# Kernel optimization log

Hardware: AMD Instinct MI355X
Metric: run time of the kernel (lower is better)

Reference implementation:

```python
import jax, jax.numpy as jnp
import numpy as np

NUM_BINS = 8
TAIL = 3.0
MBW = 1e-3
MBH = 1e-3
MD = 1e-3


def _conv(x, w, b):
    y = jax.lax.conv_general_dilated(x, w, (1, 1), 'SAME',
                                     dimension_numbers=('NCHW', 'OIHW', 'NCHW'))
    return y + b[None, :, None, None]


def _rqs_forward(x, uw, uh, ud):
    # x: [N]; uw/uh: [N,K]; ud: [N,K-1]. Linear tails at |x|>TAIL.
    K = NUM_BINS
    inside = (x >= -TAIL) & (x <= TAIL)
    pad_const = float(np.log(np.expm1(1.0 - MD)))
    ud = jnp.pad(ud, ((0, 0), (1, 1)), constant_values=pad_const)  # [N,K+1]

    w = MBW + (1.0 - MBW * K) * jax.nn.softmax(uw, axis=-1)
    cw = jnp.pad(jnp.cumsum(w, axis=-1), ((0, 0), (1, 0)))
    cw = 2.0 * TAIL * cw - TAIL
    cw = cw.at[:, 0].set(-TAIL).at[:, -1].set(TAIL)
    w = cw[:, 1:] - cw[:, :-1]

    h = MBH + (1.0 - MBH * K) * jax.nn.softmax(uh, axis=-1)
    ch = jnp.pad(jnp.cumsum(h, axis=-1), ((0, 0), (1, 0)))
    ch = 2.0 * TAIL * ch - TAIL
    ch = ch.at[:, 0].set(-TAIL).at[:, -1].set(TAIL)
    h = ch[:, 1:] - ch[:, :-1]

    d = MD + jax.nn.softplus(ud)  # [N,K+1]

    xc = jnp.clip(x, -TAIL, TAIL)
    idx = jnp.clip(jnp.sum(xc[:, None] >= cw, axis=-1) - 1, 0, K - 1)[:, None]
    g = lambda a, i: jnp.take_along_axis(a, i, axis=1)[:, 0]
    icw, iw = g(cw, idx), g(w, idx)
    ich, ih = g(ch, idx), g(h, idx)
    idl, idr = g(d, idx), g(d, idx + 1)

    delta = ih / iw
    th = (xc - icw) / iw
    th1 = 1.0 - th
    num = ih * (delta * th * th + idl * th * th1)
    den = delta + (idl + idr - 2.0 * delta) * th * th1
    y = ich + num / den
    dnum = delta * delta * (idr * th * th + 2.0 * delta * th * th1 + idl * th1 * th1)
    lad = jnp.log(dnum) - 2.0 * jnp.log(den)
    return jnp.where(inside, y, x), jnp.where(inside, lad, 0.0)


def _checker_mask(H, W):
    # parity=0: zeros at (even,even) and (odd,odd) -> mask = (i+j) % 2
    m = (np.add.outer(np.arange(H), np.arange(W)) % 2).astype(np.float32)
    return jnp.asarray(m)[None, None]


def setup_inputs() -> dict:
    key = jax.random.key(0)
    ks = jax.random.split(key, 6)
    B, C, H, W = 16, 12, 128, 128
    hid, c_out = 128, 12 * (3 * NUM_BINS - 1)  # 276
    return {
        'x': jax.random.normal(ks[0], (B, C, H, W), jnp.float32),
        'logdet': jnp.zeros((B,), jnp.float32),
        'conditioning': jax.random.normal(ks[1], (B, 4, H, W), jnp.float32),
        'w1': jax.random.normal(ks[2], (hid, C + 4, 3, 3), jnp.float32) * 0.05,
        'b1': jnp.zeros((hid,), jnp.float32),
        'w2': jax.random.normal(ks[3], (hid, hid, 3, 3), jnp.float32) * 0.05,
        'b2': jnp.zeros((hid,), jnp.float32),
        'w3': jax.random.normal(ks[4], (c_out, hid, 3, 3), jnp.float32) * 0.05,
        'b3': jnp.zeros((c_out,), jnp.float32),
    }


def reference(x, logdet, conditioning, w1, b1, w2, b2, w3, b3):
    B, C, H, W = x.shape
    K = NUM_BINS
    mask = _checker_mask(H, W)
    x_frozen = mask * x
    x_active = (1.0 - mask) * x

    inp = jnp.concatenate([x_frozen, conditioning], axis=1)
    hdn = jax.nn.relu(_conv(inp, w1, b1))
    hdn = jax.nn.relu(_conv(hdn, w2, b2))
    params = _conv(hdn, w3, b3)  # [B, C*(3K-1), H, W]

    params = params.reshape(B, C, 3 * K - 1, H, W).transpose(0, 1, 3, 4, 2)
    params = params.reshape(B * C * H * W, 3 * K - 1)
    uw, uh, ud = params[:, :K], params[:, K:2 * K], params[:, 2 * K:]

    y_flat, lad_flat = _rqs_forward(x_active.reshape(-1), uw, uh, ud)
    y = y_flat.reshape(B, C, H, W)
    x_out = x_frozen + y * (1.0 - mask)
    lad = lad_flat.reshape(B, C, H, W) * (1.0 - mask)
    return x_out, logdet + lad.sum(axis=(1, 2, 3))
```

## Files before the change

kernel.cpp:

```cpp
#include <hip/hip_runtime.h>
#include <hip/hip_bf16.h>
#include <math.h>

constexpr int B_ = 16, C_ = 12, H_ = 128, W_ = 128, HID = 128;
constexpr float TAILF = 3.0f, MBWF = 0.001f, MBHF = 0.001f, MDF = 0.001f;

typedef __attribute__((ext_vector_type(8))) short bf16x8;
typedef __attribute__((ext_vector_type(4))) short bf16x4;
typedef __attribute__((ext_vector_type(4))) float f32x4;
typedef __attribute__((ext_vector_type(2))) float f32x2;

__device__ __forceinline__ float softplusf(float v) {
    return (v > 20.f) ? v : log1pf(expf(v));
}
__device__ __forceinline__ short bf16bits(float v) {
    __hip_bfloat16 t = __float2bfloat16(v);
    return *reinterpret_cast<short*>(&t);
}
__device__ __forceinline__ float bf2f(short s) {
    __hip_bfloat16 t = *reinterpret_cast<__hip_bfloat16*>(&s);
    return __bfloat162float(t);
}

__global__ void pack_w1_kern(const float* __restrict__ w1,
                             __hip_bfloat16* __restrict__ wp) {
    int e = blockIdx.x * 256 + threadIdx.x;
    int j = e & 7, lane = (e >> 3) & 63, mt = (e >> 9) & 7;
    int chunk = e >> 12;
    int oc = mt * 16 + (lane & 15);
    int k_local = (lane >> 4) * 8 + j;
    int kpos = 2 * chunk + (k_local >> 4);
    int ic = k_local & 15;
    float v = (kpos < 9) ? w1[(oc * 16 + ic) * 9 + kpos] : 0.f;
    wp[e] = __float2bfloat16(v);
}

__global__ void pack_w2_kern(const float* __restrict__ w2,
                             __hip_bfloat16* __restrict__ wp) {
    int e = blockIdx.x * 256 + threadIdx.x;
    int j = e & 7, lane = (e >> 3) & 63, mt = (e >> 9) & 7;
    int chunk = (e >> 12) & 3, kpos = e >> 14;
    int oc = mt * 16 + (lane & 15);
    int ic = chunk * 32 + (lane >> 4) * 8 + j;
    wp[e] = __float2bfloat16(w2[(oc * 128 + ic) * 9 + kpos]);
}

__global__ void pack_w3_kern(const float* __restrict__ w3,
                             __hip_bfloat16* __restrict__ wp) {
    int e = blockIdx.x * 256 + threadIdx.x;
    int j = e & 7, lane = (e >> 3) & 63;
    int rest = e >> 9;
    int mt = rest % 24; rest /= 24;
    int chunk = rest & 3, kpos = rest >> 2;
    int ocp = mt * 16 + (lane & 15);
    int c = ocp / 24, jp = ocp % 24;
    int ic = chunk * 32 + (lane >> 4) * 8 + j;
    float v = 0.f;
    if (ocp < 288 && jp < 23)
        v = w3[((c * 23 + jp) * 128 + ic) * 9 + kpos];
    wp[e] = __float2bfloat16(v);
}

__global__ __launch_bounds__(256) void conv1_mfma_kern(
    const float* __restrict__ x, const float* __restrict__ cond,
    const __hip_bfloat16* __restrict__ wp1,
    const float* __restrict__ b1,
    __hip_bfloat16* __restrict__ h1)
{
    const int tile = blockIdx.x & 255;
    const int b    = blockIdx.x >> 8;
    const int h0 = (tile >> 4) << 3;
    const int w0 = (tile & 15) << 3;
    const int tid = threadIdx.x;
    const int wv = tid >> 6, l = tid & 63;
    const int lg = l >> 4, ln = l & 15;

    __shared__ __hip_bfloat16 sB[100 * 20];

    for (int e = tid; e < 1600; e += 256) {
        int ch = e / 100, pos = e % 100;
        int ph = pos / 10, pw = pos % 10;
        int gh = h0 + ph - 1, gw = w0 + pw - 1;
        float v = 0.f;
        if (gh >= 0 && gh < H_ && gw >= 0 && gw < W_) {
            if (ch < 12) {
                v = ((gh + gw) & 1) ? x[((b * C_ + ch) * H_ + gh) * W_ + gw] : 0.f;
            } else {
                v = cond[((b * 4 + (ch - 12)) * H_ + gh) * W_ + gw];
            }
        }
        sB[pos * 20 + ch] = __float2bfloat16(v);
    }
    __syncthreads();

    f32x4 acc[2][4];
#pragma unroll
    for (int mi = 0; mi < 2; ++mi) {
        const int ocbase = (wv * 2 + mi) * 16 + lg * 4;
#pragma unroll
        for (int nt = 0; nt < 4; ++nt)
#pragma unroll
            for (int r = 0; r < 4; ++r)
                acc[mi][nt][r] = b1[ocbase + r];
    }

#pragma unroll
    for (int chunk = 0; chunk < 5; ++chunk) {
        const int kpos = (chunk == 4) ? 8 : (2 * chunk + (lg >> 1));
        const int kh = kpos / 3, kw = kpos % 3;
        bf16x8 afr[2];
#pragma unroll
        for (int mi = 0; mi < 2; ++mi)
            afr[mi] = *reinterpret_cast<const bf16x8*>(
                &wp1[(size_t)((chunk * 8 + wv * 2 + mi) * 64 + l) * 8]);
        bf16x8 bfr[4];
#pragma unroll
        for (int nt = 0; nt < 4; ++nt) {
            int px = nt * 16 + ln;
            int pos = ((px >> 3) + kh) * 10 + (px & 7) + kw;
            bfr[nt] = *reinterpret_cast<const bf16x8*>(&sB[pos * 20 + (lg & 1) * 8]);
        }
#pragma unroll
        for (int mi = 0; mi < 2; ++mi)
#pragma unroll
            for (int nt = 0; nt < 4; ++nt)
                acc[mi][nt] = __builtin_amdgcn_mfma_f32_16x16x32_bf16(
                    afr[mi], bfr[nt], acc[mi][nt], 0, 0, 0);
    }

#pragma unroll
    for (int mi = 0; mi < 2; ++mi) {
#pragma unroll
        for (int nt = 0; nt < 4; ++nt) {
            int px = nt * 16 + ln;
            int h = h0 + (px >> 3), w = w0 + (px & 7);
            bf16x4 o;
#pragma unroll
            for (int r = 0; r < 4; ++r)
                o[r] = bf16bits(fmaxf(acc[mi][nt][r], 0.f));
            *reinterpret_cast<bf16x4*>(
                &h1[(size_t)((b * H_ + h) * W_ + w) * HID + (wv * 2 + mi) * 16 + lg * 4]) = o;
        }
    }
}

__global__ __launch_bounds__(256) void conv2_mfma_kern(
    const __hip_bfloat16* __restrict__ h1,
    const __hip_bfloat16* __restrict__ wp2,
    const float* __restrict__ b2,
    __hip_bfloat16* __restrict__ h2)
{
    const int tile = blockIdx.x & 255;
    const int b    = blockIdx.x >> 8;
    const int h0 = (tile >> 4) << 3;
    const int w0 = (tile & 15) << 3;
    const int tid = threadIdx.x;
    const int wv = tid >> 6, l = tid & 63;
    const int lg = l >> 4, ln = l & 15;

    __shared__ __hip_bfloat16 sB[100 * 40];

    f32x4 acc[2][4];
#pragma unroll
    for (int mi = 0; mi < 2; ++mi) {
        const int ocbase = (wv * 2 + mi) * 16 + lg * 4;
#pragma unroll
        for (int nt = 0; nt < 4; ++nt)
#pragma unroll
            for (int r = 0; r < 4; ++r)
                acc[mi][nt][r] = b2[ocbase + r];
    }

    for (int chunk = 0; chunk < 4; ++chunk) {
        __syncthreads();
        for (int s = tid; s < 400; s += 256) {
            int pos = s >> 2, g = s & 3;
            int ph = pos / 10, pw = pos % 10;
            int gh = h0 + ph - 1, gw = w0 + pw - 1;
            bf16x8 v = {0, 0, 0, 0, 0, 0, 0, 0};
            if (gh >= 0 && gh < H_ && gw >= 0 && gw < W_)
                v = *reinterpret_cast<const bf16x8*>(
                    &h1[(size_t)((b * H_ + gh) * W_ + gw) * HID + chunk * 32 + g * 8]);
            *reinterpret_cast<bf16x8*>(&sB[pos * 40 + g * 8]) = v;
        }
        __syncthreads();
#pragma unroll
        for (int kpos = 0; kpos < 9; ++kpos) {
            const int kh = kpos / 3, kw = kpos % 3;
            bf16x8 afr[2];
#pragma unroll
            for (int mi = 0; mi < 2; ++mi)
                afr[mi] = *reinterpret_cast<const bf16x8*>(
                    &wp2[(size_t)(((kpos * 4 + chunk) * 8 + wv * 2 + mi) * 64 + l) * 8]);
            bf16x8 bfr[4];
#pragma unroll
            for (int nt = 0; nt < 4; ++nt) {
                int px = nt * 16 + ln;
                int pos = ((px >> 3) + kh) * 10 + (px & 7) + kw;
                bfr[nt] = *reinterpret_cast<const bf16x8*>(&sB[pos * 40 + lg * 8]);
            }
#pragma unroll
            for (int mi = 0; mi < 2; ++mi)
#pragma unroll
                for (int nt = 0; nt < 4; ++nt)
                    acc[mi][nt] = __builtin_amdgcn_mfma_f32_16x16x32_bf16(
                        afr[mi], bfr[nt], acc[mi][nt], 0, 0, 0);
        }
    }
#pragma unroll
    for (int mi = 0; mi < 2; ++mi) {
#pragma unroll
        for (int nt = 0; nt < 4; ++nt) {
            int px = nt * 16 + ln;
            int h = h0 + (px >> 3), w = w0 + (px & 7);
            bf16x4 o;
#pragma unroll
            for (int r = 0; r < 4; ++r)
                o[r] = bf16bits(fmaxf(acc[mi][nt][r], 0.f));
            *reinterpret_cast<bf16x4*>(
                &h2[(size_t)((b * H_ + h) * W_ + w) * HID + (wv * 2 + mi) * 16 + lg * 4]) = o;
        }
    }
}

__global__ __launch_bounds__(256) void conv3_gemm_kern(
    const __hip_bfloat16* __restrict__ h2,
    const __hip_bfloat16* __restrict__ wp3,
    const float* __restrict__ b3,
    __hip_bfloat16* __restrict__ park, int bbase)
{
    const int mblock = blockIdx.x % 3;
    const int t2 = blockIdx.x / 3;
    const int tile = t2 & 127;
    const int b8 = t2 >> 7;
    const int b = bbase + b8;
    const int r0 = (tile >> 4) << 4;
    const int w0 = (tile & 15) << 3;
    const int tid = threadIdx.x;
    const int wv = tid >> 6, l = tid & 63;
    const int lg = l >> 4, ln = l & 15;

    __shared__ __hip_bfloat16 sB[180 * 40];

    f32x4 acc[2][4];
#pragma unroll
    for (int mi = 0; mi < 2; ++mi) {
#pragma unroll
        for (int r = 0; r < 4; ++r) {
            int ocp = mblock * 128 + (wv * 2 + mi) * 16 + lg * 4 + r;
            int c = ocp / 24, jp = ocp % 24;
            float bv = (ocp < 288 && jp < 23) ? b3[c * 23 + jp] : 0.f;
#pragma unroll
            for (int nt = 0; nt < 4; ++nt) acc[mi][nt][r] = bv;
        }
    }

    for (int chunk = 0; chunk < 4; ++chunk) {
        __syncthreads();
        for (int s = tid; s < 720; s += 256) {
            int pos = s >> 2, g = s & 3;
            int ph = pos / 10, pw = pos % 10;
            int gh = r0 + ph - 1, gw = w0 + pw - 1;
            bf16x8 v = {0, 0, 0, 0, 0, 0, 0, 0};
            if (gh >= 0 && gh < H_ && gw >= 0 && gw < W_)
                v = *reinterpret_cast<const bf16x8*>(
                    &h2[(size_t)((b * H_ + gh) * W_ + gw) * HID + chunk * 32 + g * 8]);
            *reinterpret_cast<bf16x8*>(&sB[pos * 40 + g * 8]) = v;
        }
        __syncthreads();
#pragma unroll
        for (int kpos = 0; kpos < 9; ++kpos) {
            const int kh = kpos / 3, kw = kpos % 3;
            bf16x8 afr[2];
#pragma unroll
            for (int mi = 0; mi < 2; ++mi) {
                int mtg = mblock * 8 + wv * 2 + mi;
                afr[mi] = *reinterpret_cast<const bf16x8*>(
                    &wp3[(size_t)(((kpos * 4 + chunk) * 24 + mtg) * 64 + l) * 8]);
            }
            bf16x8 bfr[4];
#pragma unroll
            for (int nt = 0; nt < 4; ++nt) {
                int px = nt * 16 + ln;
                int rr = px >> 2, a = px & 3;
                int pos = (rr + kh) * 10 + 2 * a + (rr & 1) + kw;
                bfr[nt] = *reinterpret_cast<const bf16x8*>(&sB[pos * 40 + lg * 8]);
            }
#pragma unroll
            for (int mi = 0; mi < 2; ++mi)
#pragma unroll
                for (int nt = 0; nt < 4; ++nt)
                    acc[mi][nt] = __builtin_amdgcn_mfma_f32_16x16x32_bf16(
                        afr[mi], bfr[nt], acc[mi][nt], 0, 0, 0);
        }
    }

#pragma unroll
    for (int mi = 0; mi < 2; ++mi) {
        const int ocb = mblock * 128 + (wv * 2 + mi) * 16 + lg * 4;
        if (ocb < 288) {
#pragma unroll
            for (int nt = 0; nt < 4; ++nt) {
                int px = nt * 16 + ln;
                int rr = px >> 2, a = px & 3;
                int gh = r0 + rr;
                int whalf = (w0 >> 1) + a;
                bf16x4 o;
#pragma unroll
                for (int r = 0; r < 4; ++r) o[r] = bf16bits(acc[mi][nt][r]);
                *reinterpret_cast<bf16x4*>(
                    &park[(size_t)(b8 * 8192 + gh * 64 + whalf) * 288 + ocb]) = o;
            }
        }
    }
}

__global__ __launch_bounds__(256) void rqs_kern(
    const float* __restrict__ x,
    const __hip_bfloat16* __restrict__ park,
    float* __restrict__ out, float* __restrict__ ws_lad,
    int bbase)
{
    const int tid = threadIdx.x;
    const int e = blockIdx.x * 256 + tid;
    const int c = e % 12;
    const int px_lin = e / 12;
    const int pxa = px_lin & 8191;
    const int b8 = px_lin >> 13;
    const int b = bbase + b8;
    const int gh = pxa >> 6, colhalf = pxa & 63;
    const int par = gh & 1;

    __shared__ float s_red[256];

    const __hip_bfloat16* pr = &park[(size_t)px_lin * 288 + c * 24];
    bf16x8 v0 = *reinterpret_cast<const bf16x8*>(pr);
    bf16x8 v1 = *reinterpret_cast<const bf16x8*>(pr + 8);
    bf16x8 v2 = *reinterpret_cast<const bf16x8*>(pr + 16);
    float p[23];
#pragma unroll
    for (int j = 0; j < 8; ++j) p[j] = bf2f(v0[j]);
#pragma unroll
    for (int j = 0; j < 8; ++j) p[8 + j] = bf2f(v1[j]);
#pragma unroll
    for (int j = 0; j < 7; ++j) p[16 + j] = bf2f(v2[j]);

    float mw = p[0];
#pragma unroll
    for (int j = 1; j < 8; ++j) mw = fmaxf(mw, p[j]);
    float ew[8], sw = 0.f;
#pragma unroll
    for (int j = 0; j < 8; ++j) { ew[j] = expf(p[j] - mw); sw += ew[j]; }
    float mh = p[8];
#pragma unroll
    for (int j = 1; j < 8; ++j) mh = fmaxf(mh, p[8 + j]);
    float eh[8], sh = 0.f;
#pragma unroll
    for (int j = 0; j < 8; ++j) { eh[j] = expf(p[8 + j] - mh); sh += eh[j]; }

    float cwv[9], chv[9];
    cwv[0] = -TAILF; chv[0] = -TAILF;
    float cum_w = 0.f, cum_h = 0.f;
    const float invsw = 1.f / sw, invsh = 1.f / sh;
#pragma unroll
    for (int j = 0; j < 8; ++j) {
        cum_w += MBWF + (1.f - MBWF * 8.f) * ew[j] * invsw;
        cum_h += MBHF + (1.f - MBHF * 8.f) * eh[j] * invsh;
        cwv[j + 1] = 2.f * TAILF * cum_w - TAILF;
        chv[j + 1] = 2.f * TAILF * cum_h - TAILF;
    }
    cwv[8] = TAILF; chv[8] = TAILF;

    float dv[9];
    dv[0] = 1.f; dv[8] = 1.f;
#pragma unroll
    for (int j = 1; j < 8; ++j) dv[j] = MDF + softplusf(p[15 + j]);

    const int base = ((b * C_ + c) * H_ + gh) * W_ + 2 * colhalf;
    f32x2 xp = *reinterpret_cast<const f32x2*>(&x[base]);
    const float xa = par ? xp[1] : xp[0];
    const float xf = par ? xp[0] : xp[1];

    const float xc = fminf(fmaxf(xa, -TAILF), TAILF);
    int cnt = 0;
#pragma unroll
    for (int i = 0; i < 9; ++i) cnt += (xc >= cwv[i]) ? 1 : 0;
    int idx = cnt - 1;
    idx = idx < 0 ? 0 : (idx > 7 ? 7 : idx);

    float icw = cwv[0], iwd = cwv[1] - cwv[0];
    float ich = chv[0], ihd = chv[1] - chv[0];
    float idl = dv[0], idr = dv[1];
#pragma unroll
    for (int i = 1; i < 8; ++i) {
        if (idx == i) {
            icw = cwv[i]; iwd = cwv[i + 1] - cwv[i];
            ich = chv[i]; ihd = chv[i + 1] - chv[i];
            idl = dv[i];  idr = dv[i + 1];
        }
    }
    const float delta = ihd / iwd;
    const float th  = (xc - icw) / iwd;
    const float th1 = 1.f - th;
    const float num = ihd * (delta * th * th + idl * th * th1);
    const float den = delta + (idl + idr - 2.f * delta) * th * th1;
    float y = ich + num / den;
    const float dnum = delta * delta *
        (idr * th * th + 2.f * delta * th * th1 + idl * th1 * th1);
    float lad = logf(dnum) - 2.f * logf(den);
    const bool inside = (xa >= -TAILF) && (xa <= TAILF);
    y = inside ? y : xa;
    lad = inside ? lad : 0.f;

    f32x2 op;
    op[par] = y; op[par ^ 1] = xf;
    *reinterpret_cast<f32x2*>(&out[base]) = op;

    s_red[tid] = lad;
    __syncthreads();
    for (int s = 128; s > 0; s >>= 1) {
        if (tid < s) s_red[tid] += s_red[tid + s];
        __syncthreads();
    }
    if (tid == 0) ws_lad[blockIdx.x] = s_red[0];
}

__global__ void logdet_reduce_kern(const float* __restrict__ ws_lad,
                                   const float* __restrict__ logdet_in,
                                   float* __restrict__ out)
{
    int b = threadIdx.x;
    if (b < B_) {
        float s = logdet_in[b];
        const float* p = &ws_lad[(b >> 3) * 3072 + (b & 7) * 384];
        for (int i = 0; i < 384; ++i) s += p[i];
        out[(size_t)B_ * C_ * H_ * W_ + b] = s;
    }
}

extern "C" void kernel_launch(void* const* d_in, const int* in_sizes, int n_in,
                              void* d_out, int out_size, void* d_ws, size_t ws_size,
                              hipStream_t stream) {
    const float* x    = (const float*)d_in[0];
    const float* ld   = (const float*)d_in[1];
    const float* cond = (const float*)d_in[2];
    const float* w1   = (const float*)d_in[3];
    const float* b1   = (const float*)d_in[4];
    const float* w2   = (const float*)d_in[5];
    const float* b2   = (const float*)d_in[6];
    const float* w3   = (const float*)d_in[7];
    const float* b3   = (const float*)d_in[8];
    float* out = (float*)d_out;

    const size_t NPIX = (size_t)B_ * H_ * W_;
    __hip_bfloat16* h1 = (__hip_bfloat16*)d_ws;
    __hip_bfloat16* h2 = h1 + NPIX * HID;
    const size_t PARK_HALF = (size_t)8 * 8192 * 288;
    __hip_bfloat16* park0 = (__hip_bfloat16*)d_ws;
    __hip_bfloat16* park1 = park0 + PARK_HALF;
    float* ws_lad = (float*)((char*)d_ws + (((size_t)128 << 20) - 32768));
    __hip_bfloat16* wp2 = (__hip_bfloat16*)d_out;
    __hip_bfloat16* wp1 = (__hip_bfloat16*)((char*)d_out + (1u << 19));
    __hip_bfloat16* wp3 = (__hip_bfloat16*)((char*)d_out + (1u << 20));

    hipLaunchKernelGGL(pack_w1_kern, dim3(80), dim3(256), 0, stream, w1, wp1);
    hipLaunchKernelGGL(pack_w2_kern, dim3(576), dim3(256), 0, stream, w2, wp2);
    hipLaunchKernelGGL(pack_w3_kern, dim3(1728), dim3(256), 0, stream, w3, wp3);
    hipLaunchKernelGGL(conv1_mfma_kern, dim3(16 * 256), dim3(256), 0, stream,
                       x, cond, wp1, b1, h1);
    hipLaunchKernelGGL(conv2_mfma_kern, dim3(16 * 256), dim3(256), 0, stream,
                       h1, wp2, b2, h2);
    hipLaunchKernelGGL(conv3_gemm_kern, dim3(8 * 128 * 3), dim3(256), 0, stream,
                       h2, wp3, b3, park0, 0);
    hipLaunchKernelGGL(conv3_gemm_kern, dim3(8 * 128 * 3), dim3(256), 0, stream,
                       h2, wp3, b3, park1, 8);
    hipLaunchKernelGGL(rqs_kern, dim3(3072), dim3(256), 0, stream,
                       x, park0, out, ws_lad, 0);
    hipLaunchKernelGGL(rqs_kern, dim3(3072), dim3(256), 0, stream,
                       x, park1, out, ws_lad + 3072, 8);
    hipLaunchKernelGGL(logdet_reduce_kern, dim3(1), dim3(64), 0, stream,
                       ws_lad, ld, out);
}
```

Before: 320.0 us.

## Enlarge conv2/conv3 output tiles and switch parameter buffer to channel-major layout

Conv2 now computes a 16x8 pixel tile per block, with each wave covering 4 output-channel tiles by 4 pixel tiles, so every staged halo and weight fragment feeds more MFMAs. Conv3 moves to 16x16 pixel tiles, drops the padded 288-channel layout for 276 channels in 18 M-tiles, and pads the LDS row stride to 44 to reduce bank conflicts. The parameter buffer is stored channel-major so each RQS thread reads 23 coalesced scalars instead of strided vectors, and the logdet reduction indexing is updated to match. The trade-offs are higher register and LDS use per block, fewer blocks in flight, and scalar, less-vectorized parameter stores in the conv3 epilogue.

```diff
diff --git a/kernel.cpp b/kernel.cpp
--- a/kernel.cpp
+++ b/kernel.cpp
@@ -50,14 +50,11 @@
     int e = blockIdx.x * 256 + threadIdx.x;
     int j = e & 7, lane = (e >> 3) & 63;
     int rest = e >> 9;
-    int mt = rest % 24; rest /= 24;
+    int mt = rest % 18; rest /= 18;
     int chunk = rest & 3, kpos = rest >> 2;
     int ocp = mt * 16 + (lane & 15);
-    int c = ocp / 24, jp = ocp % 24;
     int ic = chunk * 32 + (lane >> 4) * 8 + j;
-    float v = 0.f;
-    if (ocp < 288 && jp < 23)
-        v = w3[((c * 23 + jp) * 128 + ic) * 9 + kpos];
+    float v = (ocp < 276) ? w3[(ocp * 128 + ic) * 9 + kpos] : 0.f;
     wp[e] = __float2bfloat16(v);
 }
 
@@ -150,20 +147,21 @@
     const float* __restrict__ b2,
     __hip_bfloat16* __restrict__ h2)
 {
-    const int tile = blockIdx.x & 255;
-    const int b    = blockIdx.x >> 8;
-    const int h0 = (tile >> 4) << 3;
+    const int tile = blockIdx.x & 127;
+    const int b    = blockIdx.x >> 7;
+    const int h0 = (tile >> 4) << 4;
     const int w0 = (tile & 15) << 3;
     const int tid = threadIdx.x;
     const int wv = tid >> 6, l = tid & 63;
     const int lg = l >> 4, ln = l & 15;
-
-    __shared__ __hip_bfloat16 sB[100 * 40];
-
-    f32x4 acc[2][4];
-#pragma unroll
-    for (int mi = 0; mi < 2; ++mi) {
-        const int ocbase = (wv * 2 + mi) * 16 + lg * 4;
+    const int mh = wv >> 1, nh = wv & 1;
+
+    __shared__ __hip_bfloat16 sB[180 * 40];
+
+    f32x4 acc[4][4];
+#pragma unroll
+    for (int mi = 0; mi < 4; ++mi) {
+        const int ocbase = (mh * 4 + mi) * 16 + lg * 4;
 #pragma unroll
         for (int nt = 0; nt < 4; ++nt)
 #pragma unroll
@@ -173,7 +171,7 @@
 
     for (int chunk = 0; chunk < 4; ++chunk) {
         __syncthreads();
-        for (int s = tid; s < 400; s += 256) {
+        for (int s = tid; s < 720; s += 256) {
             int pos = s >> 2, g = s & 3;
             int ph = pos / 10, pw = pos % 10;
             int gh = h0 + ph - 1, gw = w0 + pw - 1;
@@ -187,20 +185,20 @@
 #pragma unroll
         for (int kpos = 0; kpos < 9; ++kpos) {
             const int kh = kpos / 3, kw = kpos % 3;
-            bf16x8 afr[2];
-#pragma unroll
-            for (int mi = 0; mi < 2; ++mi)
+            bf16x8 afr[4];
+#pragma unroll
+            for (int mi = 0; mi < 4; ++mi)
                 afr[mi] = *reinterpret_cast<const bf16x8*>(
-                    &wp2[(size_t)(((kpos * 4 + chunk) * 8 + wv * 2 + mi) * 64 + l) * 8]);
+                    &wp2[(size_t)(((kpos * 4 + chunk) * 8 + mh * 4 + mi) * 64 + l) * 8]);
             bf16x8 bfr[4];
 #pragma unroll
             for (int nt = 0; nt < 4; ++nt) {
-                int px = nt * 16 + ln;
+                int px = (nh * 4 + nt) * 16 + ln;
                 int pos = ((px >> 3) + kh) * 10 + (px & 7) + kw;
                 bfr[nt] = *reinterpret_cast<const bf16x8*>(&sB[pos * 40 + lg * 8]);
             }
 #pragma unroll
-            for (int mi = 0; mi < 2; ++mi)
+            for (int mi = 0; mi < 4; ++mi)
 #pragma unroll
                 for (int nt = 0; nt < 4; ++nt)
                     acc[mi][nt] = __builtin_amdgcn_mfma_f32_16x16x32_bf16(
@@ -208,17 +206,17 @@
         }
     }
 #pragma unroll
-    for (int mi = 0; mi < 2; ++mi) {
+    for (int mi = 0; mi < 4; ++mi) {
 #pragma unroll
         for (int nt = 0; nt < 4; ++nt) {
-            int px = nt * 16 + ln;
+            int px = (nh * 4 + nt) * 16 + ln;
             int h = h0 + (px >> 3), w = w0 + (px & 7);
             bf16x4 o;
 #pragma unroll
             for (int r = 0; r < 4; ++r)
                 o[r] = bf16bits(fmaxf(acc[mi][nt][r], 0.f));
             *reinterpret_cast<bf16x4*>(
-                &h2[(size_t)((b * H_ + h) * W_ + w) * HID + (wv * 2 + mi) * 16 + lg * 4]) = o;
+                &h2[(size_t)((b * H_ + h) * W_ + w) * HID + (mh * 4 + mi) * 16 + lg * 4]) = o;
         }
     }
 }
@@ -231,25 +229,25 @@
 {
     const int mblock = blockIdx.x % 3;
     const int t2 = blockIdx.x / 3;
-    const int tile = t2 & 127;
-    const int b8 = t2 >> 7;
+    const int tile = t2 & 63;
+    const int b8 = t2 >> 6;
     const int b = bbase + b8;
-    const int r0 = (tile >> 4) << 4;
-    const int w0 = (tile & 15) << 3;
+    const int r0 = (tile >> 3) << 4;
+    const int w0 = (tile & 7) << 4;
     const int tid = threadIdx.x;
     const int wv = tid >> 6, l = tid & 63;
     const int lg = l >> 4, ln = l & 15;
-
-    __shared__ __hip_bfloat16 sB[180 * 40];
-
-    f32x4 acc[2][4];
-#pragma unroll
-    for (int mi = 0; mi < 2; ++mi) {
+    const int mh = wv >> 1, nh = wv & 1;
+
+    __shared__ __hip_bfloat16 sB[324 * 44];
+
+    f32x4 acc[3][4];
+#pragma unroll
+    for (int mi = 0; mi < 3; ++mi) {
 #pragma unroll
         for (int r = 0; r < 4; ++r) {
-            int ocp = mblock * 128 + (wv * 2 + mi) * 16 + lg * 4 + r;
-            int c = ocp / 24, jp = ocp % 24;
-            float bv = (ocp < 288 && jp < 23) ? b3[c * 23 + jp] : 0.f;
+            int ocp = (mblock * 6 + mh * 3 + mi) * 16 + lg * 4 + r;
+            float bv = (ocp < 276) ? b3[ocp] : 0.f;
 #pragma unroll
             for (int nt = 0; nt < 4; ++nt) acc[mi][nt][r] = bv;
         }
@@ -257,59 +255,54 @@
 
     for (int chunk = 0; chunk < 4; ++chunk) {
         __syncthreads();
-        for (int s = tid; s < 720; s += 256) {
+        for (int s = tid; s < 1296; s += 256) {
             int pos = s >> 2, g = s & 3;
-            int ph = pos / 10, pw = pos % 10;
+            int ph = pos / 18, pw = pos % 18;
             int gh = r0 + ph - 1, gw = w0 + pw - 1;
             bf16x8 v = {0, 0, 0, 0, 0, 0, 0, 0};
             if (gh >= 0 && gh < H_ && gw >= 0 && gw < W_)
                 v = *reinterpret_cast<const bf16x8*>(
                     &h2[(size_t)((b * H_ + gh) * W_ + gw) * HID + chunk * 32 + g * 8]);
-            *reinterpret_cast<bf16x8*>(&sB[pos * 40 + g * 8]) = v;
+            *reinterpret_cast<bf16x8*>(&sB[pos * 44 + g * 8]) = v;
         }
         __syncthreads();
 #pragma unroll
         for (int kpos = 0; kpos < 9; ++kpos) {
             const int kh = kpos / 3, kw = kpos % 3;
-            bf16x8 afr[2];
-#pragma unroll
-            for (int mi = 0; mi < 2; ++mi) {
-                int mtg = mblock * 8 + wv * 2 + mi;
-                afr[mi] = *reinterpret_cast<const bf16x8*>(
-                    &wp3[(size_t)(((kpos * 4 + chunk) * 24 + mtg) * 64 + l) * 8]);
+            bf16x8 bfr[4];
+#pragma unroll
+            for (int nt = 0; nt < 4; ++nt) {
+                int px = (nh * 4 + nt) * 16 + ln;
+                int rr = px >> 3, a = px & 7;
+                int pos = (rr + kh) * 18 + 2 * a + (rr & 1) + kw;
+                bfr[nt] = *reinterpret_cast<const bf16x8*>(&sB[pos * 44 + lg * 8]);
             }
-            bf16x8 bfr[4];
-#pragma unroll
-            for (int nt = 0; nt < 4; ++nt) {
-                int px = nt * 16 + ln;
-                int rr = px >> 2, a = px & 3;
-                int pos = (rr + kh) * 10 + 2 * a + (rr & 1) + kw;
-                bfr[nt] = *reinterpret_cast<const bf16x8*>(&sB[pos * 40 + lg * 8]);
-            }
-#pragma unroll
-            for (int mi = 0; mi < 2; ++mi)
+#pragma unroll
+            for (int mi = 0; mi < 3; ++mi) {
+                bf16x8 afr = *reinterpret_cast<const bf16x8*>(
+                    &wp3[(size_t)(((kpos * 4 + chunk) * 18 + mblock * 6 + mh * 3 + mi) * 64 + l) * 8]);
 #pragma unroll
                 for (int nt = 0; nt < 4; ++nt)
                     acc[mi][nt] = __builtin_amdgcn_mfma_f32_16x16x32_bf16(
-                        afr[mi], bfr[nt], acc[mi][nt], 0, 0, 0);
-        }
-    }
-
-#pragma unroll
-    for (int mi = 0; mi < 2; ++mi) {
-        const int ocb = mblock * 128 + (wv * 2 + mi) * 16 + lg * 4;
-        if (ocb < 288) {
+                        afr, bfr[nt], acc[mi][nt], 0, 0, 0);
+            }
+        }
+    }
+
+#pragma unroll
+    for (int mi = 0; mi < 3; ++mi) {
+        const int ocb = (mblock * 6 + mh * 3 + mi) * 16 + lg * 4;
+        if (ocb < 276) {
 #pragma unroll
             for (int nt = 0; nt < 4; ++nt) {
-                int px = nt * 16 + ln;
-                int rr = px >> 2, a = px & 3;
+                int px = (nh * 4 + nt) * 16 + ln;
+                int rr = px >> 3, a = px & 7;
                 int gh = r0 + rr;
-                int whalf = (w0 >> 1) + a;
-                bf16x4 o;
-#pragma unroll
-                for (int r = 0; r < 4; ++r) o[r] = bf16bits(acc[mi][nt][r]);
-                *reinterpret_cast<bf16x4*>(
-                    &park[(size_t)(b8 * 8192 + gh * 64 + whalf) * 288 + ocb]) = o;
+                int ag = (w0 >> 1) + a;
+                int pxa = b8 * 8192 + gh * 64 + ag;
+#pragma unroll
+                for (int r = 0; r < 4; ++r)
+                    park[(size_t)(ocb + r) * 65536 + pxa] = __float2bfloat16(acc[mi][nt][r]);
             }
         }
     }
@@ -322,28 +315,20 @@
     int bbase)
 {
     const int tid = threadIdx.x;
-    const int e = blockIdx.x * 256 + tid;
-    const int c = e % 12;
-    const int px_lin = e / 12;
-    const int pxa = px_lin & 8191;
-    const int b8 = px_lin >> 13;
+    const int c = blockIdx.x >> 8;
+    const int pxa = ((blockIdx.x & 255) << 8) | tid;
+    const int b8 = pxa >> 13;
     const int b = bbase + b8;
-    const int gh = pxa >> 6, colhalf = pxa & 63;
+    const int gh = (pxa >> 6) & 127;
+    const int a = pxa & 63;
     const int par = gh & 1;
 
     __shared__ float s_red[256];
 
-    const __hip_bfloat16* pr = &park[(size_t)px_lin * 288 + c * 24];
-    bf16x8 v0 = *reinterpret_cast<const bf16x8*>(pr);
-    bf16x8 v1 = *reinterpret_cast<const bf16x8*>(pr + 8);
-    bf16x8 v2 = *reinterpret_cast<const bf16x8*>(pr + 16);
     float p[23];
 #pragma unroll
-    for (int j = 0; j < 8; ++j) p[j] = bf2f(v0[j]);
-#pragma unroll
-    for (int j = 0; j < 8; ++j) p[8 + j] = bf2f(v1[j]);
-#pragma unroll
-    for (int j = 0; j < 7; ++j) p[16 + j] = bf2f(v2[j]);
+    for (int j = 0; j < 23; ++j)
+        p[j] = __bfloat162float(park[(size_t)(c * 23 + j) * 65536 + pxa]);
 
     float mw = p[0];
 #pragma unroll
@@ -376,7 +361,7 @@
 #pragma unroll
     for (int j = 1; j < 8; ++j) dv[j] = MDF + softplusf(p[15 + j]);
 
-    const int base = ((b * C_ + c) * H_ + gh) * W_ + 2 * colhalf;
+    const int base = ((b * C_ + c) * H_ + gh) * W_ + 2 * a;
     f32x2 xp = *reinterpret_cast<const f32x2*>(&x[base]);
     const float xa = par ? xp[1] : xp[0];
     const float xf = par ? xp[0] : xp[1];
@@ -431,9 +416,11 @@
 {
     int b = threadIdx.x;
     if (b < B_) {
+        int h = b >> 3, b8 = b & 7;
+        const float* p = &ws_lad[h * 3072 + b8 * 32];
         float s = logdet_in[b];
-        const float* p = &ws_lad[(b >> 3) * 3072 + (b & 7) * 384];
-        for (int i = 0; i < 384; ++i) s += p[i];
+        for (int c = 0; c < 12; ++c)
+            for (int i = 0; i < 32; ++i) s += p[c * 256 + i];
         out[(size_t)B_ * C_ * H_ * W_ + b] = s;
     }
 }
@@ -455,7 +442,7 @@
     const size_t NPIX = (size_t)B_ * H_ * W_;
     __hip_bfloat16* h1 = (__hip_bfloat16*)d_ws;
     __hip_bfloat16* h2 = h1 + NPIX * HID;
-    const size_t PARK_HALF = (size_t)8 * 8192 * 288;
+    const size_t PARK_HALF = (size_t)288 * 65536;
     __hip_bfloat16* park0 = (__hip_bfloat16*)d_ws;
     __hip_bfloat16* park1 = park0 + PARK_HALF;
     float* ws_lad = (float*)((char*)d_ws + (((size_t)128 << 20) - 32768));
@@ -465,14 +452,14 @@
 
     hipLaunchKernelGGL(pack_w1_kern, dim3(80), dim3(256), 0, stream, w1, wp1);
     hipLaunchKernelGGL(pack_w2_kern, dim3(576), dim3(256), 0, stream, w2, wp2);
-    hipLaunchKernelGGL(pack_w3_kern, dim3(1728), dim3(256), 0, stream, w3, wp3);
+    hipLaunchKernelGGL(pack_w3_kern, dim3(1296), dim3(256), 0, stream, w3, wp3);
     hipLaunchKernelGGL(conv1_mfma_kern, dim3(16 * 256), dim3(256), 0, stream,
                        x, cond, wp1, b1, h1);
-    hipLaunchKernelGGL(conv2_mfma_kern, dim3(16 * 256), dim3(256), 0, stream,
+    hipLaunchKernelGGL(conv2_mfma_kern, dim3(16 * 128), dim3(256), 0, stream,
                        h1, wp2, b2, h2);
-    hipLaunchKernelGGL(conv3_gemm_kern, dim3(8 * 128 * 3), dim3(256), 0, stream,
+    hipLaunchKernelGGL(conv3_gemm_kern, dim3(8 * 64 * 3), dim3(256), 0, stream,
                        h2, wp3, b3, park0, 0);
-    hipLaunchKernelGGL(conv3_gemm_kern, dim3(8 * 128 * 3), dim3(256), 0, stream,
+    hipLaunchKernelGGL(conv3_gemm_kern, dim3(8 * 64 * 3), dim3(256), 0, stream,
                        h2, wp3, b3, park1, 8);
     hipLaunchKernelGGL(rqs_kern, dim3(3072), dim3(256), 0, stream,
                        x, park0, out, ws_lad, 0);
```

Measured after the change: 417.6 us. 1.31x slower.

## Double-buffer conv2 input tile and prefetch weight fragments in registers

Applied to the files above, without the earlier changes.

Conv2 now keeps two LDS buffers for the input halo tile. It issues the global loads for the next 32-channel chunk before the MFMA loop over the current chunk, so load latency overlaps compute. Weight fragments for the next kernel position are also loaded one step ahead, and the per-thread address math is hoisted out of the chunk loop. The cost is twice the LDS footprint, more registers held live, and an extra barrier per chunk, any of which could reduce occupancy.

```diff
diff --git a/kernel.cpp b/kernel.cpp
--- a/kernel.cpp
+++ b/kernel.cpp
@@ -158,7 +158,22 @@
     const int wv = tid >> 6, l = tid & 63;
     const int lg = l >> 4, ln = l & 15;
 
-    __shared__ __hip_bfloat16 sB[100 * 40];
+    __shared__ __hip_bfloat16 sB[2][100 * 40];
+
+    const int s0 = tid, s1 = tid + 256;
+    const int pos0 = s0 >> 2, g0 = s0 & 3;
+    const int gh0 = h0 + pos0 / 10 - 1, gw0 = w0 + pos0 % 10 - 1;
+    const bool ok0 = (gh0 >= 0 && gh0 < H_ && gw0 >= 0 && gw0 < W_);
+    const size_t idx0 = ok0 ? ((size_t)((b * H_ + gh0) * W_ + gw0) * HID + g0 * 8) : 0;
+    const int lofs0 = pos0 * 40 + g0 * 8;
+    const bool has1 = (s1 < 400);
+    const int pos1 = s1 >> 2, g1 = s1 & 3;
+    const int gh1 = h0 + pos1 / 10 - 1, gw1 = w0 + pos1 % 10 - 1;
+    const bool ok1 = has1 && (gh1 >= 0 && gh1 < H_ && gw1 >= 0 && gw1 < W_);
+    const size_t idx1 = ok1 ? ((size_t)((b * H_ + gh1) * W_ + gw1) * HID + g1 * 8) : 0;
+    const int lofs1 = pos1 * 40 + g1 * 8;
+
+    const bf16x8 zz = {0, 0, 0, 0, 0, 0, 0, 0};
 
     f32x4 acc[2][4];
 #pragma unroll
@@ -171,42 +186,58 @@
                 acc[mi][nt][r] = b2[ocbase + r];
     }
 
-    for (int chunk = 0; chunk < 4; ++chunk) {
-        __syncthreads();
-        for (int s = tid; s < 400; s += 256) {
-            int pos = s >> 2, g = s & 3;
-            int ph = pos / 10, pw = pos % 10;
-            int gh = h0 + ph - 1, gw = w0 + pw - 1;
-            bf16x8 v = {0, 0, 0, 0, 0, 0, 0, 0};
-            if (gh >= 0 && gh < H_ && gw >= 0 && gw < W_)
-                v = *reinterpret_cast<const bf16x8*>(
-                    &h1[(size_t)((b * H_ + gh) * W_ + gw) * HID + chunk * 32 + g * 8]);
-            *reinterpret_cast<bf16x8*>(&sB[pos * 40 + g * 8]) = v;
-        }
-        __syncthreads();
+    {
+        bf16x8 r0 = ok0 ? *reinterpret_cast<const bf16x8*>(&h1[idx0]) : zz;
+        bf16x8 r1 = ok1 ? *reinterpret_cast<const bf16x8*>(&h1[idx1]) : zz;
+        *reinterpret_cast<bf16x8*>(&sB[0][lofs0]) = r0;
+        if (has1) *reinterpret_cast<bf16x8*>(&sB[0][lofs1]) = r1;
+    }
+    __syncthreads();
+
+    for (int c = 0; c < 4; ++c) {
+        const int cur = c & 1;
+        bf16x8 n0 = zz, n1 = zz;
+        if (c < 3) {
+            if (ok0) n0 = *reinterpret_cast<const bf16x8*>(&h1[idx0 + (size_t)(c + 1) * 32]);
+            if (ok1) n1 = *reinterpret_cast<const bf16x8*>(&h1[idx1 + (size_t)(c + 1) * 32]);
+        }
+        bf16x8 a0 = *reinterpret_cast<const bf16x8*>(
+            &wp2[(size_t)(((0 * 4 + c) * 8 + wv * 2 + 0) * 64 + l) * 8]);
+        bf16x8 a1 = *reinterpret_cast<const bf16x8*>(
+            &wp2[(size_t)(((0 * 4 + c) * 8 + wv * 2 + 1) * 64 + l) * 8]);
 #pragma unroll
         for (int kpos = 0; kpos < 9; ++kpos) {
+            const bf16x8 c0 = a0, c1 = a1;
+            if (kpos < 8) {
+                a0 = *reinterpret_cast<const bf16x8*>(
+                    &wp2[(size_t)((((kpos + 1) * 4 + c) * 8 + wv * 2 + 0) * 64 + l) * 8]);
+                a1 = *reinterpret_cast<const bf16x8*>(
+                    &wp2[(size_t)((((kpos + 1) * 4 + c) * 8 + wv * 2 + 1) * 64 + l) * 8]);
+            }
             const int kh = kpos / 3, kw = kpos % 3;
-            bf16x8 afr[2];
-#pragma unroll
-            for (int mi = 0; mi < 2; ++mi)
-                afr[mi] = *reinterpret_cast<const bf16x8*>(
-                    &wp2[(size_t)(((kpos * 4 + chunk) * 8 + wv * 2 + mi) * 64 + l) * 8]);
             bf16x8 bfr[4];
 #pragma unroll
             for (int nt = 0; nt < 4; ++nt) {
                 int px = nt * 16 + ln;
                 int pos = ((px >> 3) + kh) * 10 + (px & 7) + kw;
-                bfr[nt] = *reinterpret_cast<const bf16x8*>(&sB[pos * 40 + lg * 8]);
-            }
-#pragma unroll
-            for (int mi = 0; mi < 2; ++mi)
-#pragma unroll
-                for (int nt = 0; nt < 4; ++nt)
-                    acc[mi][nt] = __builtin_amdgcn_mfma_f32_16x16x32_bf16(
-                        afr[mi], bfr[nt], acc[mi][nt], 0, 0, 0);
-        }
-    }
+                bfr[nt] = *reinterpret_cast<const bf16x8*>(&sB[cur][pos * 40 + lg * 8]);
+            }
+#pragma unroll
+            for (int nt = 0; nt < 4; ++nt) {
+                acc[0][nt] = __builtin_amdgcn_mfma_f32_16x16x32_bf16(
+                    c0, bfr[nt], acc[0][nt], 0, 0, 0);
+                acc[1][nt] = __builtin_amdgcn_mfma_f32_16x16x32_bf16(
+                    c1, bfr[nt], acc[1][nt], 0, 0, 0);
+            }
+        }
+        if (c < 3) {
+            __syncthreads();
+            *reinterpret_cast<bf16x8*>(&sB[cur ^ 1][lofs0]) = n0;
+            if (has1) *reinterpret_cast<bf16x8*>(&sB[cur ^ 1][lofs1]) = n1;
+            __syncthreads();
+        }
+    }
+
 #pragma unroll
     for (int mi = 0; mi < 2; ++mi) {
 #pragma unroll
```

Result: no change. 320.6 us (+0.2%).

## Load conv2/conv3 input fragments directly from global memory instead of LDS staging

Applied to the files above, without the earlier changes.

Conv2 and conv3 no longer stage each input-channel chunk into shared memory with barriers. Each lane now loads its MFMA B fragment straight from global memory, relying on L1/L2 caches to absorb the 9x re-reads across kernel positions. This drops the LDS footprint and the syncthreads, which may raise occupancy, but it adds many more global load instructions and exposes their latency. The three weight-packing kernels are also merged into one launch to cut launch overhead.

```diff
diff --git a/kernel.cpp b/kernel.cpp
--- a/kernel.cpp
+++ b/kernel.cpp
@@ -22,43 +22,44 @@
     return __bfloat162float(t);
 }
 
-__global__ void pack_w1_kern(const float* __restrict__ w1,
-                             __hip_bfloat16* __restrict__ wp) {
-    int e = blockIdx.x * 256 + threadIdx.x;
-    int j = e & 7, lane = (e >> 3) & 63, mt = (e >> 9) & 7;
-    int chunk = e >> 12;
-    int oc = mt * 16 + (lane & 15);
-    int k_local = (lane >> 4) * 8 + j;
-    int kpos = 2 * chunk + (k_local >> 4);
-    int ic = k_local & 15;
-    float v = (kpos < 9) ? w1[(oc * 16 + ic) * 9 + kpos] : 0.f;
-    wp[e] = __float2bfloat16(v);
-}
-
-__global__ void pack_w2_kern(const float* __restrict__ w2,
-                             __hip_bfloat16* __restrict__ wp) {
-    int e = blockIdx.x * 256 + threadIdx.x;
-    int j = e & 7, lane = (e >> 3) & 63, mt = (e >> 9) & 7;
-    int chunk = (e >> 12) & 3, kpos = e >> 14;
-    int oc = mt * 16 + (lane & 15);
-    int ic = chunk * 32 + (lane >> 4) * 8 + j;
-    wp[e] = __float2bfloat16(w2[(oc * 128 + ic) * 9 + kpos]);
-}
-
-__global__ void pack_w3_kern(const float* __restrict__ w3,
-                             __hip_bfloat16* __restrict__ wp) {
-    int e = blockIdx.x * 256 + threadIdx.x;
-    int j = e & 7, lane = (e >> 3) & 63;
-    int rest = e >> 9;
-    int mt = rest % 24; rest /= 24;
-    int chunk = rest & 3, kpos = rest >> 2;
-    int ocp = mt * 16 + (lane & 15);
-    int c = ocp / 24, jp = ocp % 24;
-    int ic = chunk * 32 + (lane >> 4) * 8 + j;
-    float v = 0.f;
-    if (ocp < 288 && jp < 23)
-        v = w3[((c * 23 + jp) * 128 + ic) * 9 + kpos];
-    wp[e] = __float2bfloat16(v);
+__global__ void pack_all_kern(const float* __restrict__ w1,
+                              const float* __restrict__ w2,
+                              const float* __restrict__ w3,
+                              __hip_bfloat16* __restrict__ wp1,
+                              __hip_bfloat16* __restrict__ wp2,
+                              __hip_bfloat16* __restrict__ wp3) {
+    const int blk = blockIdx.x;
+    if (blk < 80) {
+        int e = blk * 256 + threadIdx.x;
+        int j = e & 7, lane = (e >> 3) & 63, mt = (e >> 9) & 7;
+        int chunk = e >> 12;
+        int oc = mt * 16 + (lane & 15);
+        int k_local = (lane >> 4) * 8 + j;
+        int kpos = 2 * chunk + (k_local >> 4);
+        int ic = k_local & 15;
+        float v = (kpos < 9) ? w1[(oc * 16 + ic) * 9 + kpos] : 0.f;
+        wp1[e] = __float2bfloat16(v);
+    } else if (blk < 656) {
+        int e = (blk - 80) * 256 + threadIdx.x;
+        int j = e & 7, lane = (e >> 3) & 63, mt = (e >> 9) & 7;
+        int chunk = (e >> 12) & 3, kpos = e >> 14;
+        int oc = mt * 16 + (lane & 15);
+        int ic = chunk * 32 + (lane >> 4) * 8 + j;
+        wp2[e] = __float2bfloat16(w2[(oc * 128 + ic) * 9 + kpos]);
+    } else {
+        int e = (blk - 656) * 256 + threadIdx.x;
+        int j = e & 7, lane = (e >> 3) & 63;
+        int rest = e >> 9;
+        int mt = rest % 24; rest /= 24;
+        int chunk = rest & 3, kpos = rest >> 2;
+        int ocp = mt * 16 + (lane & 15);
+        int c = ocp / 24, jp = ocp % 24;
+        int ic = chunk * 32 + (lane >> 4) * 8 + j;
+        float v = 0.f;
+        if (ocp < 288 && jp < 23)
+            v = w3[((c * 23 + jp) * 128 + ic) * 9 + kpos];
+        wp3[e] = __float2bfloat16(v);
+    }
 }
 
 __global__ __launch_bounds__(256) void conv1_mfma_kern(
@@ -158,8 +159,6 @@
     const int wv = tid >> 6, l = tid & 63;
     const int lg = l >> 4, ln = l & 15;
 
-    __shared__ __hip_bfloat16 sB[100 * 40];
-
     f32x4 acc[2][4];
 #pragma unroll
     for (int mi = 0; mi < 2; ++mi) {
@@ -171,19 +170,10 @@
                 acc[mi][nt][r] = b2[ocbase + r];
     }
 
+    const int pcol = ln & 7;
+    const bf16x8 zz = {0, 0, 0, 0, 0, 0, 0, 0};
+
     for (int chunk = 0; chunk < 4; ++chunk) {
-        __syncthreads();
-        for (int s = tid; s < 400; s += 256) {
-            int pos = s >> 2, g = s & 3;
-            int ph = pos / 10, pw = pos % 10;
-            int gh = h0 + ph - 1, gw = w0 + pw - 1;
-            bf16x8 v = {0, 0, 0, 0, 0, 0, 0, 0};
-            if (gh >= 0 && gh < H_ && gw >= 0 && gw < W_)
-                v = *reinterpret_cast<const bf16x8*>(
-                    &h1[(size_t)((b * H_ + gh) * W_ + gw) * HID + chunk * 32 + g * 8]);
-            *reinterpret_cast<bf16x8*>(&sB[pos * 40 + g * 8]) = v;
-        }
-        __syncthreads();
 #pragma unroll
         for (int kpos = 0; kpos < 9; ++kpos) {
             const int kh = kpos / 3, kw = kpos % 3;
@@ -195,9 +185,13 @@
             bf16x8 bfr[4];
 #pragma unroll
             for (int nt = 0; nt < 4; ++nt) {
-                int px = nt * 16 + ln;
-                int pos = ((px >> 3) + kh) * 10 + (px & 7) + kw;
-                bfr[nt] = *reinterpret_cast<const bf16x8*>(&sB[pos * 40 + lg * 8]);
+                const int gh = h0 + nt * 2 + (ln >> 3) + kh - 1;
+                const int gw = w0 + pcol + kw - 1;
+                bf16x8 v = zz;
+                if (((unsigned)gh < (unsigned)H_) && ((unsigned)gw < (unsigned)W_))
+                    v = *reinterpret_cast<const bf16x8*>(
+                        &h1[(size_t)((b * H_ + gh) * W_ + gw) * HID + chunk * 32 + lg * 8]);
+                bfr[nt] = v;
             }
 #pragma unroll
             for (int mi = 0; mi < 2; ++mi)
@@ -207,6 +201,7 @@
                         afr[mi], bfr[nt], acc[mi][nt], 0, 0, 0);
         }
     }
+
 #pragma unroll
     for (int mi = 0; mi < 2; ++mi) {
 #pragma unroll
@@ -218,7 +213,7 @@
             for (int r = 0; r < 4; ++r)
                 o[r] = bf16bits(fmaxf(acc[mi][nt][r], 0.f));
             *reinterpret_cast<bf16x4*>(
-                &h2[(size_t)((b * H_ + h) * W_ + w) * HID + (wv * 2 + mi) * 16 + lg * 4]) = o;
+                &h2[(size_t)((b * H_ + h) * W_ + w) * HID + (mi + wv * 2) * 16 + lg * 4]) = o;
         }
     }
 }
@@ -240,8 +235,6 @@
     const int wv = tid >> 6, l = tid & 63;
     const int lg = l >> 4, ln = l & 15;
 
-    __shared__ __hip_bfloat16 sB[180 * 40];
-
     f32x4 acc[2][4];
 #pragma unroll
     for (int mi = 0; mi < 2; ++mi) {
@@ -255,19 +248,18 @@
         }
     }
 
+    int prow[4], pc[4];
+#pragma unroll
+    for (int nt = 0; nt < 4; ++nt) {
+        int px = nt * 16 + ln;
+        int rr = px >> 2, a = px & 3;
+        prow[nt] = rr;
+        pc[nt] = 2 * a + (rr & 1);
+    }
+
+    const bf16x8 zz = {0, 0, 0, 0, 0, 0, 0, 0};
+
     for (int chunk = 0; chunk < 4; ++chunk) {
-        __syncthreads();
-        for (int s = tid; s < 720; s += 256) {
-            int pos = s >> 2, g = s & 3;
-            int ph = pos / 10, pw = pos % 10;
-            int gh = r0 + ph - 1, gw = w0 + pw - 1;
-            bf16x8 v = {0, 0, 0, 0, 0, 0, 0, 0};
-            if (gh >= 0 && gh < H_ && gw >= 0 && gw < W_)
-                v = *reinterpret_cast<const bf16x8*>(
-                    &h2[(size_t)((b * H_ + gh) * W_ + gw) * HID + chunk * 32 + g * 8]);
-            *reinterpret_cast<bf16x8*>(&sB[pos * 40 + g * 8]) = v;
-        }
-        __syncthreads();
 #pragma unroll
         for (int kpos = 0; kpos < 9; ++kpos) {
             const int kh = kpos / 3, kw = kpos % 3;
@@ -281,10 +273,13 @@
             bf16x8 bfr[4];
 #pragma unroll
             for (int nt = 0; nt < 4; ++nt) {
-                int px = nt * 16 + ln;
-                int rr = px >> 2, a = px & 3;
-                int pos = (rr + kh) * 10 + 2 * a + (rr & 1) + kw;
-                bfr[nt] = *reinterpret_cast<const bf16x8*>(&sB[pos * 40 + lg * 8]);
+                const int gh = r0 + prow[nt] + kh - 1;
+                const int gw = w0 + pc[nt] + kw - 1;
+                bf16x8 v = zz;
+                if (((unsigned)gh < (unsigned)H_) && ((unsigned)gw < (unsigned)W_))
+                    v = *reinterpret_cast<const bf16x8*>(
+                        &h2[(size_t)((b * H_ + gh) * W_ + gw) * HID + chunk * 32 + lg * 8]);
+                bfr[nt] = v;
             }
 #pragma unroll
             for (int mi = 0; mi < 2; ++mi)
@@ -463,9 +458,8 @@
     __hip_bfloat16* wp1 = (__hip_bfloat16*)((char*)d_out + (1u << 19));
     __hip_bfloat16* wp3 = (__hip_bfloat16*)((char*)d_out + (1u << 20));
 
-    hipLaunchKernelGGL(pack_w1_kern, dim3(80), dim3(256), 0, stream, w1, wp1);
-    hipLaunchKernelGGL(pack_w2_kern, dim3(576), dim3(256), 0, stream, w2, wp2);
-    hipLaunchKernelGGL(pack_w3_kern, dim3(1728), dim3(256), 0, stream, w3, wp3);
+    hipLaunchKernelGGL(pack_all_kern, dim3(2384), dim3(256), 0, stream,
+                       w1, w2, w3, wp1, wp2, wp3);
     hipLaunchKernelGGL(conv1_mfma_kern, dim3(16 * 256), dim3(256), 0, stream,
                        x, cond, wp1, b1, h1);
     hipLaunchKernelGGL(conv2_mfma_kern, dim3(16 * 256), dim3(256), 0, stream,
```

New measurement: 816.6 us. +155.2%, slower.
